# Kernel optimization log

Hardware: AMD Instinct MI355X
Metric: run time of the kernel (lower is better)

The kernel has to match this reference:

```python
import jax, jax.numpy as jnp
import numpy as np

EPS = 1e-7  # K.epsilon()
ROUTINGS = 3

def squash(v):
    # v: [..., dim_capsule]
    s2 = jnp.sum(jnp.square(v), axis=-1, keepdims=True)
    scale = s2 / (1.0 + s2) / jnp.sqrt(s2 + EPS)
    return scale * v

def setup_inputs() -> dict:
    key = jax.random.key(0)
    k1, k2 = jax.random.split(key)
    B, IN_CAPS, IN_DIM = 256, 1152, 8
    NUM_CAPS, DIM_CAPS = 10, 16
    inputs = jax.random.normal(k1, (B, IN_CAPS, IN_DIM), dtype=jnp.float32)
    W = jax.random.normal(k2, (NUM_CAPS, IN_CAPS, DIM_CAPS, IN_DIM), dtype=jnp.float32) * 0.05
    return {"inputs": inputs, "W": W}

def reference(inputs, W):
    # inputs: [B, I, Q]; W: [J, I, P, Q]
    # inputs_hat[b,j,i,p] = sum_q W[j,i,p,q] * inputs[b,i,q]
    inputs_hat = jnp.einsum('jipq,biq->bjip', W, inputs)  # [B, J, I, P]
    B, J, I, P = inputs_hat.shape
    b = jnp.zeros((B, J, I), dtype=inputs_hat.dtype)
    outputs = None
    for r in range(ROUTINGS):
        c = jax.nn.softmax(b, axis=1)                      # over num_capsule J
        s = jnp.einsum('bji,bjip->bjp', c, inputs_hat)     # [B, J, P]
        outputs = squash(s)
        if r < ROUTINGS - 1:
            b = b + jnp.einsum('bjp,bjip->bji', outputs, inputs_hat)
    return outputs
```

## Files before the change

### kernel.cpp

```cpp
#include <hip/hip_runtime.h>

typedef _Float16 h2 __attribute__((ext_vector_type(2)));
typedef _Float16 h8 __attribute__((ext_vector_type(8)));
typedef float f4 __attribute__((ext_vector_type(4)));

#define BB 256
#define II 1152
#define QQ 8
#define JJ 10
#define PP 16

#define BT 16
#define IT 8
#define NBT (BB / BT)
#define NIT (II / IT)
#define XRH 72
#define WTILE (IT * PP * QQ)

#define NW (JJ * II * PP * QQ)
#define NX (BB * II * QQ)
#define NS (BB * JJ * PP)
#define LOG2E 1.4426950408889634f

template <int CTRL>
__device__ __forceinline__ float dpp_add(float v) {
    int s = __builtin_bit_cast(int, v);
    int t = __builtin_amdgcn_update_dpp(0, s, CTRL, 0xF, 0xF, true);
    return v + __builtin_bit_cast(float, t);
}
__device__ __forceinline__ float row_sum16(float v) {
    v = dpp_add<0xB1>(v);
    v = dpp_add<0x4E>(v);
    v = dpp_add<0x124>(v);
    v = dpp_add<0x128>(v);
    return v;
}
template <int CTRL>
__device__ __forceinline__ h2 dpp_add_pk(h2 v) {
    int s = __builtin_bit_cast(int, v);
    int t = __builtin_amdgcn_update_dpp(0, s, CTRL, 0xF, 0xF, true);
    return v + __builtin_bit_cast(h2, t);
}
__device__ __forceinline__ h2 row_sum16_pk(h2 v) {
    v = dpp_add_pk<0xB1>(v);
    v = dpp_add_pk<0x4E>(v);
    v = dpp_add_pk<0x124>(v);
    v = dpp_add_pk<0x128>(v);
    return v;
}

__device__ __forceinline__ float dot8(h8 w, h8 x) {
    h2 w0 = __builtin_shufflevector(w, w, 0, 1), w1 = __builtin_shufflevector(w, w, 2, 3);
    h2 w2 = __builtin_shufflevector(w, w, 4, 5), w3 = __builtin_shufflevector(w, w, 6, 7);
    h2 x0 = __builtin_shufflevector(x, x, 0, 1), x1 = __builtin_shufflevector(x, x, 2, 3);
    h2 x2 = __builtin_shufflevector(x, x, 4, 5), x3 = __builtin_shufflevector(x, x, 6, 7);
    float acc = __builtin_amdgcn_fdot2(w0, x0, 0.0f, false);
    acc = __builtin_amdgcn_fdot2(w1, x1, acc, false);
    acc = __builtin_amdgcn_fdot2(w2, x2, acc, false);
    acc = __builtin_amdgcn_fdot2(w3, x3, acc, false);
    return acc;
}

__global__ __launch_bounds__(256) void prep_kernel(
    const float* __restrict__ X, const float* __restrict__ W,
    _Float16* __restrict__ Xh, _Float16* __restrict__ Wh,
    _Float16* __restrict__ XT,
    float* __restrict__ S)
{
    const int g = blockIdx.x * 256 + threadIdx.x;
    const int stride = gridDim.x * 256;
    typedef _Float16 h4 __attribute__((ext_vector_type(4)));
    for (int k = g; k < NW / 4; k += stride) {
        const float4 f = ((const float4*)W)[k];
        h4 o = { (_Float16)f.x, (_Float16)f.y, (_Float16)f.z, (_Float16)f.w };
        ((h4*)Wh)[k] = o;
    }
    for (int k = g; k < NX / 4; k += stride) {
        const float4 f = ((const float4*)X)[k];
        h4 o = { (_Float16)f.x, (_Float16)f.y, (_Float16)f.z, (_Float16)f.w };
        ((h4*)Xh)[k] = o;
        const int e0 = k * 4;
        const int b  = e0 / (II * QQ);
        const int r  = e0 - b * (II * QQ);
        const int i  = r >> 3;
        const int q  = r & 7;
        *(h4*)(XT + ((size_t)i * BB + b) * QQ + q) = o;
    }
    const float4 z = {0.f, 0.f, 0.f, 0.f};
    for (int k = g; k < 3 * NS / 4; k += stride) ((float4*)S)[k] = z;
}

__global__ __launch_bounds__(256) void s0_mfma_kernel(
    const _Float16* __restrict__ XT, const _Float16* __restrict__ Wh,
    float* __restrict__ S0)
{
    const int wid  = blockIdx.x * 4 + (threadIdx.x >> 6);
    const int lane = threadIdx.x & 63;
    const int bt  = wid / 80;
    const int rem = wid % 80;
    const int j   = rem >> 3;
    const int kc  = rem & 7;
    const int b0  = bt * 16;
    const int m    = lane & 15;
    const int quad = lane >> 4;
    const int ib   = kc * 144;

    const _Float16* ax = XT + ((size_t)(ib + quad) * BB + b0 + m) * QQ;
    const _Float16* bw = Wh + (((size_t)j * II + ib + quad) * PP + m) * QQ;

    f4 acc = {0.f, 0.f, 0.f, 0.f};
    for (int t = 0; t < 36; ++t) {
        const h8 a = *(const h8*)ax;
        const h8 b = *(const h8*)bw;
        acc = __builtin_amdgcn_mfma_f32_16x16x32_f16(a, b, acc, 0, 0, 0);
        ax += (size_t)4 * BB * QQ;
        bw += (size_t)4 * PP * QQ;
    }
#pragma unroll
    for (int r = 0; r < 4; ++r)
        atomicAdd(&S0[((size_t)(b0 + quad * 4 + r) * JJ + j) * PP + m], 0.1f * acc[r]);
}

template <int MODE>
__global__ __launch_bounds__(256) void vv_kernel(
    const float* __restrict__ S, float* __restrict__ V0raw,
    float* __restrict__ VV)
{
    const int idx = blockIdx.x * 256 + threadIdx.x;
    const float s = S[idx];
    const float n2 = row_sum16(s * s);
    const float sc = n2 * __builtin_amdgcn_rcpf(1.0f + n2)
                        * __builtin_amdgcn_rsqf(n2 + 1e-7f);
    const float v = s * sc;
    if (MODE == 0) {
        V0raw[idx] = v;
        VV[idx] = v * LOG2E;
    } else {
        VV[idx] = (v + V0raw[idx]) * LOG2E;
    }
}

__global__ __launch_bounds__(256, 4) void pass_kernel(
    const _Float16* __restrict__ Xh,
    const _Float16* __restrict__ Wh,
    const float* __restrict__ VV,
    float* __restrict__ Sout)
{
    __shared__ _Float16 ws[JJ * WTILE];
    __shared__ _Float16 xs[BT * XRH];

    const int L  = blockIdx.x;
    const int xc = L & 7;
    const int k8 = L >> 3;
    const int bt = 2 * xc + (k8 & 1);
    const int it = k8 >> 1;
    const int b0 = bt * BT;
    const int i0 = it * IT;
    const int tid = threadIdx.x;

    {
        const size_t jstride = (size_t)II * PP * QQ;
        const _Float16* wsrc = Wh + (size_t)i0 * PP * QQ;
#pragma unroll
        for (int k = 0; k < 5; ++k) {
            const int c = tid + k * 256;
            const int j = c >> 7;
            const int r = c & 127;
            *(h8*)(ws + j * WTILE + r * 8) = *(const h8*)(wsrc + j * jstride + r * 8);
        }
        if (tid < 128) {
            const int xb = tid >> 3;
            const int xr = tid & 7;
            *(h8*)(xs + xb * XRH + xr * 8) =
                *(const h8*)(Xh + ((size_t)(b0 + xb) * II + i0) * QQ + xr * 8);
        }
    }
    __syncthreads();

    const int b_l = tid >> 4;
    const int p   = tid & 15;
    const int b   = b0 + b_l;

    h2 vvpk[5];
#pragma unroll
    for (int jp = 0; jp < JJ; jp += 2) {
        const float v0 = VV[((size_t)b * JJ + jp) * PP + p];
        const float v1 = VV[((size_t)b * JJ + jp + 1) * PP + p];
        vvpk[jp >> 1] = __builtin_bit_cast(h2, __builtin_amdgcn_cvt_pkrtz(v0, v1));
    }

    float sacc[JJ];
#pragma unroll
    for (int j = 0; j < JJ; ++j) sacc[j] = 0.0f;

    const _Float16* wb = ws + p * QQ;
    const _Float16* xb = xs + b_l * XRH;

#pragma unroll
    for (int i = 0; i < IT; ++i) {
        const h8 x8 = *(const h8*)(xb + i * QQ);

        float h[JJ];
#pragma unroll
        for (int j = 0; j < JJ; ++j)
            h[j] = dot8(*(const h8*)(wb + j * WTILE + i * PP * QQ), x8);

        float e[JJ];
#pragma unroll
        for (int jp = 0; jp < JJ; jp += 2) {
            const h2 hp = __builtin_bit_cast(h2,
                __builtin_amdgcn_cvt_pkrtz(h[jp], h[jp + 1]));
            const h2 r = row_sum16_pk(vvpk[jp >> 1] * hp);
            e[jp]     = __builtin_amdgcn_exp2f((float)r.x);
            e[jp + 1] = __builtin_amdgcn_exp2f((float)r.y);
        }
        float a0 = (e[0] + e[1]) + (e[2] + e[3]);
        float a1 = (e[4] + e[5]) + (e[6] + e[7]);
        const float sum = (a0 + a1) + (e[8] + e[9]);
        const float inv = __builtin_amdgcn_rcpf(sum);
#pragma unroll
        for (int j = 0; j < JJ; ++j) sacc[j] += (e[j] * inv) * h[j];
    }

#pragma unroll
    for (int j = 0; j < JJ; ++j)
        atomicAdd(&Sout[((size_t)b * JJ + j) * PP + p], sacc[j]);
}

__global__ __launch_bounds__(256) void squash_out_kernel(const float* __restrict__ S,
                                                         float* __restrict__ V)
{
    const int idx = blockIdx.x * blockDim.x + threadIdx.x;
    if (idx >= BB * JJ) return;
    const float4* sp = (const float4*)(S + idx * PP);
    float4 a = sp[0], b4 = sp[1], c4 = sp[2], d4 = sp[3];
    float s2 = a.x * a.x + a.y * a.y + a.z * a.z + a.w * a.w +
               b4.x * b4.x + b4.y * b4.y + b4.z * b4.z + b4.w * b4.w +
               c4.x * c4.x + c4.y * c4.y + c4.z * c4.z + c4.w * c4.w +
               d4.x * d4.x + d4.y * d4.y + d4.z * d4.z + d4.w * d4.w;
    const float scale = s2 / (1.0f + s2) / sqrtf(s2 + 1e-7f);
    a.x *= scale; a.y *= scale; a.z *= scale; a.w *= scale;
    b4.x *= scale; b4.y *= scale; b4.z *= scale; b4.w *= scale;
    c4.x *= scale; c4.y *= scale; c4.z *= scale; c4.w *= scale;
    d4.x *= scale; d4.y *= scale; d4.z *= scale; d4.w *= scale;
    float4* vp = (float4*)(V + idx * PP);
    vp[0] = a; vp[1] = b4; vp[2] = c4; vp[3] = d4;
}

extern "C" void kernel_launch(void* const* d_in, const int* in_sizes, int n_in,
                              void* d_out, int out_size, void* d_ws, size_t ws_size,
                              hipStream_t stream)
{
    const float* X = (const float*)d_in[0];
    const float* W = (const float*)d_in[1];
    float* out = (float*)d_out;

    _Float16* Xh = (_Float16*)d_ws;
    _Float16* Wh = Xh + NX;
    _Float16* XT = Wh + NW;
    float* S0 = (float*)(XT + NX);
    float* S1 = S0 + NS;
    float* S2 = S1 + NS;
    float* V0raw = S2 + NS;
    float* VV1   = V0raw + NS;
    float* VV2   = VV1 + NS;

    const int grid  = NBT * NIT;
    const int vgrid = NS / 256;

    prep_kernel<<<1024, 256, 0, stream>>>(X, W, Xh, Wh, XT, S0);
    s0_mfma_kernel<<<320, 256, 0, stream>>>(XT, Wh, S0);
    vv_kernel<0><<<vgrid, 256, 0, stream>>>(S0, V0raw, VV1);
    pass_kernel<<<grid, 256, 0, stream>>>(Xh, Wh, VV1, S1);
    vv_kernel<1><<<vgrid, 256, 0, stream>>>(S1, V0raw, VV2);
    pass_kernel<<<grid, 256, 0, stream>>>(Xh, Wh, VV2, S2);
    squash_out_kernel<<<10, 256, 0, stream>>>(S2, out);
}
```

Before: 132.3 us.

## Process two batch rows per thread to reuse W fragments from LDS

Doubles the batch tile to 32 so each thread handles two batch entries, loading the ten W fragments from shared memory once per input capsule and reusing them for both. This halves the number of blocks and W tile loads per batch and cuts LDS reads per FLOP. In exchange it raises register pressure, sets the inner loop to unroll 1, and drops the previous interleaved block-to-tile mapping.

New measurement: 140.9 us. 6.5% more time.

```diff
diff --git a/kernel.cpp b/kernel.cpp
--- a/kernel.cpp
+++ b/kernel.cpp
@@ -10,7 +10,7 @@
 #define JJ 10
 #define PP 16
 
-#define BT 16
+#define BT 32
 #define IT 8
 #define NBT (BB / BT)
 #define NIT (II / IT)
@@ -150,10 +150,8 @@
     __shared__ _Float16 xs[BT * XRH];
 
     const int L  = blockIdx.x;
-    const int xc = L & 7;
-    const int k8 = L >> 3;
-    const int bt = 2 * xc + (k8 & 1);
-    const int it = k8 >> 1;
+    const int bt = L & 7;
+    const int it = L >> 3;
     const int b0 = bt * BT;
     const int i0 = it * IT;
     const int tid = threadIdx.x;
@@ -168,7 +166,7 @@
             const int r = c & 127;
             *(h8*)(ws + j * WTILE + r * 8) = *(const h8*)(wsrc + j * jstride + r * 8);
         }
-        if (tid < 128) {
+        {
             const int xb = tid >> 3;
             const int xr = tid & 7;
             *(h8*)(xs + xb * XRH + xr * 8) =
@@ -179,52 +177,86 @@
 
     const int b_l = tid >> 4;
     const int p   = tid & 15;
-    const int b   = b0 + b_l;
-
-    h2 vvpk[5];
+    const int bA  = b0 + b_l;
+    const int bB  = bA + 16;
+
+    h2 vvA[5], vvB[5];
 #pragma unroll
     for (int jp = 0; jp < JJ; jp += 2) {
-        const float v0 = VV[((size_t)b * JJ + jp) * PP + p];
-        const float v1 = VV[((size_t)b * JJ + jp + 1) * PP + p];
-        vvpk[jp >> 1] = __builtin_bit_cast(h2, __builtin_amdgcn_cvt_pkrtz(v0, v1));
-    }
-
-    float sacc[JJ];
-#pragma unroll
-    for (int j = 0; j < JJ; ++j) sacc[j] = 0.0f;
-
-    const _Float16* wb = ws + p * QQ;
-    const _Float16* xb = xs + b_l * XRH;
-
-#pragma unroll
+        vvA[jp >> 1] = __builtin_bit_cast(h2, __builtin_amdgcn_cvt_pkrtz(
+            VV[((size_t)bA * JJ + jp) * PP + p],
+            VV[((size_t)bA * JJ + jp + 1) * PP + p]));
+        vvB[jp >> 1] = __builtin_bit_cast(h2, __builtin_amdgcn_cvt_pkrtz(
+            VV[((size_t)bB * JJ + jp) * PP + p],
+            VV[((size_t)bB * JJ + jp + 1) * PP + p]));
+    }
+
+    float saccA[JJ], saccB[JJ];
+#pragma unroll
+    for (int j = 0; j < JJ; ++j) { saccA[j] = 0.0f; saccB[j] = 0.0f; }
+
+    const _Float16* wb  = ws + p * QQ;
+    const _Float16* xbA = xs + b_l * XRH;
+    const _Float16* xbB = xs + (b_l + 16) * XRH;
+
+#pragma unroll 1
     for (int i = 0; i < IT; ++i) {
-        const h8 x8 = *(const h8*)(xb + i * QQ);
-
-        float h[JJ];
+        h8 wf[JJ];
 #pragma unroll
         for (int j = 0; j < JJ; ++j)
-            h[j] = dot8(*(const h8*)(wb + j * WTILE + i * PP * QQ), x8);
-
-        float e[JJ];
-#pragma unroll
-        for (int jp = 0; jp < JJ; jp += 2) {
-            const h2 hp = __builtin_bit_cast(h2,
-                __builtin_amdgcn_cvt_pkrtz(h[jp], h[jp + 1]));
-            const h2 r = row_sum16_pk(vvpk[jp >> 1] * hp);
-            e[jp]     = __builtin_amdgcn_exp2f((float)r.x);
-            e[jp + 1] = __builtin_amdgcn_exp2f((float)r.y);
+            wf[j] = *(const h8*)(wb + j * WTILE + i * PP * QQ);
+
+        const h8 xA = *(const h8*)(xbA + i * QQ);
+        const h8 xB = *(const h8*)(xbB + i * QQ);
+
+        {
+            float h[JJ];
+#pragma unroll
+            for (int j = 0; j < JJ; ++j) h[j] = dot8(wf[j], xA);
+            float e[JJ];
+#pragma unroll
+            for (int jp = 0; jp < JJ; jp += 2) {
+                const h2 hp = __builtin_bit_cast(h2,
+                    __builtin_amdgcn_cvt_pkrtz(h[jp], h[jp + 1]));
+                const h2 r = row_sum16_pk(vvA[jp >> 1] * hp);
+                e[jp]     = __builtin_amdgcn_exp2f((float)r.x);
+                e[jp + 1] = __builtin_amdgcn_exp2f((float)r.y);
+            }
+            float a0 = (e[0] + e[1]) + (e[2] + e[3]);
+            float a1 = (e[4] + e[5]) + (e[6] + e[7]);
+            const float sum = (a0 + a1) + (e[8] + e[9]);
+            const float inv = __builtin_amdgcn_rcpf(sum);
+#pragma unroll
+            for (int j = 0; j < JJ; ++j) saccA[j] += (e[j] * inv) * h[j];
         }
-        float a0 = (e[0] + e[1]) + (e[2] + e[3]);
-        float a1 = (e[4] + e[5]) + (e[6] + e[7]);
-        const float sum = (a0 + a1) + (e[8] + e[9]);
-        const float inv = __builtin_amdgcn_rcpf(sum);
-#pragma unroll
-        for (int j = 0; j < JJ; ++j) sacc[j] += (e[j] * inv) * h[j];
+        {
+            float h[JJ];
+#pragma unroll
+            for (int j = 0; j < JJ; ++j) h[j] = dot8(wf[j], xB);
+            float e[JJ];
+#pragma unroll
+            for (int jp = 0; jp < JJ; jp += 2) {
+                const h2 hp = __builtin_bit_cast(h2,
+                    __builtin_amdgcn_cvt_pkrtz(h[jp], h[jp + 1]));
+                const h2 r = row_sum16_pk(vvB[jp >> 1] * hp);
+                e[jp]     = __builtin_amdgcn_exp2f((float)r.x);
+                e[jp + 1] = __builtin_amdgcn_exp2f((float)r.y);
+            }
+            float a0 = (e[0] + e[1]) + (e[2] + e[3]);
+            float a1 = (e[4] + e[5]) + (e[6] + e[7]);
+            const float sum = (a0 + a1) + (e[8] + e[9]);
+            const float inv = __builtin_amdgcn_rcpf(sum);
+#pragma unroll
+            for (int j = 0; j < JJ; ++j) saccB[j] += (e[j] * inv) * h[j];
+        }
     }
 
 #pragma unroll
     for (int j = 0; j < JJ; ++j)
-        atomicAdd(&Sout[((size_t)b * JJ + j) * PP + p], sacc[j]);
+        atomicAdd(&Sout[((size_t)bA * JJ + j) * PP + p], saccA[j]);
+#pragma unroll
+    for (int j = 0; j < JJ; ++j)
+        atomicAdd(&Sout[((size_t)bB * JJ + j) * PP + p], saccB[j]);
 }
 
 __global__ __launch_bounds__(256) void squash_out_kernel(const float* __restrict__ S,
```
